# Performance work log

Measured on AMD Instinct MI355X. Metric: run time of the kernel, lower is better.

The kernel has to match this reference:

```python
import jax, jax.numpy as jnp
import numpy as np

N_ELEMENTS = 64  # StructureElementLayer(n_elements=64)


def setup_inputs() -> dict:
    key = jax.random.key(0)
    k1, k2 = jax.random.split(key)
    # x: [N, C, T, V] skeleton sequence (batch, coord channels, time, joints)
    x = jax.random.normal(k1, (256, 3, 256, 25), dtype=jnp.float32)
    # StructureElementLayer parameters (torch.rand init / ones*3 init)
    centres = jax.random.uniform(k2, (N_ELEMENTS, 2), dtype=jnp.float32)
    sharpness = jnp.ones((N_ELEMENTS, 2), dtype=jnp.float32) * 3.0
    return {"x": x, "centres": centres, "sharpness": sharpness}


def _mst_deaths(D):
    """Dim-0 Vietoris-Rips persistence deaths == MST edge weights (Prim's algorithm).

    D: [n, n] symmetric distance matrix. Returns [n-1] finite death values
    (births are all 0; the single essential (0, inf) pair contributes
    exp(-inf)=0 to the structure-element layer and is dropped).
    """
    n = D.shape[0]
    in_tree = jnp.zeros((n,), dtype=bool).at[0].set(True)
    dist = D[0]  # min distance from each node to the current tree

    def step(carry, _):
        in_tree, dist = carry
        d = jnp.where(in_tree, jnp.inf, dist)
        j = jnp.argmin(d)
        w = d[j]
        in_tree = in_tree.at[j].set(True)
        dist = jnp.minimum(dist, D[j])
        return (in_tree, dist), w

    (_, _), deaths = jax.lax.scan(step, (in_tree, dist), None, length=n - 1)
    return deaths


def _forward(x, centres, sharpness):
    xm = x.mean(1)                                  # [N, T, V]
    diff = xm[..., :, None] - xm[..., None, :]      # [N, T, V, V] pairwise joint diffs
    diff = diff.mean(-3)                            # [N, V, V]
    feat = jnp.linalg.norm(diff, axis=1)            # [N, V]  (torch.norm(., 2, dim=1))
    feat = (feat - feat.min()) / (feat.max() - feat.min())
    # Euclidean distance matrix of the N points in V-dim space (grad-safe sqrt)
    sq = jnp.sum(feat * feat, axis=1)
    D2 = sq[:, None] + sq[None, :] - 2.0 * (feat @ feat.T)
    D2 = jnp.maximum(D2, 0.0)
    D = jnp.where(D2 > 0.0, jnp.sqrt(jnp.where(D2 > 0.0, D2, 1.0)), 0.0)
    deaths = _mst_deaths(D)                         # [N-1]
    diag = jnp.stack([jnp.zeros_like(deaths), deaths], axis=-1)  # [N-1, 2] (birth, death)
    # StructureElementLayer: sum_i exp(-sum_d (p_id - c_kd)^2 * s_kd^2)
    d2 = (diag[:, None, :] - centres[None, :, :]) ** 2            # [N-1, K, 2]
    out = jnp.exp(-(d2 * (sharpness ** 2)).sum(-1)).sum(0)        # [K]
    return out


def reference(x, centres, sharpness):
    return _forward(x, centres, sharpness)
```

## Files before the change

kernel.cpp:

```cpp
#include <hip/hip_runtime.h>
#include <hip/hip_fp16.h>


#define WS_M    0
#define WS_MM   25600
#define WS_D16  65536

__global__ void k_mean(const float* __restrict__ x, float* __restrict__ m) {
    const int n = blockIdx.x;
    const int tid = threadIdx.x;
    __shared__ float sums[25];
    if (tid < 25) sums[tid] = 0.0f;
    __syncthreads();
    if (tid < 200) {
        const float* base = x + (long)n * 19200 + 4 * tid;
        float a0 = 0.f, a1 = 0.f, a2 = 0.f, a3 = 0.f;
        #pragma unroll
        for (int i = 0; i < 24; ++i) {
            float4 v = *reinterpret_cast<const float4*>(base + 800 * i);
            a0 += v.x; a1 += v.y; a2 += v.z; a3 += v.w;
        }
        const int v0 = (4 * tid) % 25;
        atomicAdd(&sums[v0], a0);
        atomicAdd(&sums[(v0 + 1) % 25], a1);
        atomicAdd(&sums[(v0 + 2) % 25], a2);
        atomicAdd(&sums[(v0 + 3) % 25], a3);
    }
    __syncthreads();
    if (tid < 25) m[n * 25 + tid] = sums[tid] * (1.0f / 768.0f);
}

__global__ void __launch_bounds__(256) k_dist(const float* __restrict__ m,
                                              unsigned short* __restrict__ D16,
                                              unsigned int* __restrict__ mm) {
    __shared__ float mS[6400];
    __shared__ float featS[6400];
    __shared__ unsigned int bmin, bmax;
    const int i = blockIdx.x;
    const int t = threadIdx.x;
    if (t == 0) { bmin = 0x7F800000u; bmax = 0u; }
    #pragma unroll
    for (int it = 0; it < 7; ++it) {
        int o = it * 256 + t;
        if (o < 1600) reinterpret_cast<float4*>(mS)[o] =
            reinterpret_cast<const float4*>(m)[o];
    }
    __syncthreads();
    float r[25];
    #pragma unroll
    for (int v = 0; v < 25; ++v) r[v] = mS[t * 25 + v];
    float S1 = 0.f, S2 = 0.f;
    #pragma unroll
    for (int v = 0; v < 25; ++v) { S1 += r[v]; S2 += r[v] * r[v]; }
    float fmn = 1e30f, fmx = -1e30f;
    #pragma unroll
    for (int w = 0; w < 25; ++w) {
        float q = S2 - 2.f * r[w] * S1 + 25.f * r[w] * r[w];
        q = fmaxf(q, 0.f);
        float f = sqrtf(q);
        featS[t * 25 + w] = f;
        fmn = fminf(fmn, f); fmx = fmaxf(fmx, f);
    }
    if (i == 0) {
        atomicMin(&bmin, __float_as_uint(fmn));
        atomicMax(&bmax, __float_as_uint(fmx));
    }
    __syncthreads();
    if (i == 0 && t == 0) { mm[0] = bmin; mm[1] = bmax; }
    float fi[25];
    #pragma unroll
    for (int v = 0; v < 25; ++v) fi[v] = featS[i * 25 + v];
    float s = 0.f;
    #pragma unroll
    for (int v = 0; v < 25; ++v) { float d = fi[v] - featS[t * 25 + v]; s += d * d; }
    D16[i * 256 + t] = __half_as_ushort(__float2half(s));
}

#define DSTR 264

__global__ void __launch_bounds__(256) k_mst(const unsigned short* __restrict__ D16g,
                                             const unsigned int* __restrict__ mm,
                                             const float* __restrict__ centres,
                                             const float* __restrict__ sharp,
                                             float* __restrict__ out) {
    __shared__ __align__(16) unsigned short Dl[256 * DSTR];
    __shared__ __align__(8) unsigned char compA[256];
    __shared__ unsigned char parent[256];
    __shared__ unsigned int compKey[256];
    __shared__ float deaths[256];
    __shared__ unsigned int dcount;
    __shared__ float outpart[256];
    const int tid = threadIdx.x;

    {
        const uint4* src = reinterpret_cast<const uint4*>(D16g);
        #pragma unroll
        for (int it = 0; it < 32; ++it) {
            const int flat = it * 256 + tid;
            const int r = flat >> 5, c = flat & 31;
            *reinterpret_cast<uint4*>(reinterpret_cast<char*>(Dl) + r * (DSTR * 2) + c * 16)
                = src[flat];
        }
    }
    compA[tid] = (unsigned char)tid;
    if (tid == 0) dcount = 0;
    __syncthreads();

    const int i = tid;
    const unsigned int ihi = (unsigned int)i << 8;
    const uint4* rowv = reinterpret_cast<const uint4*>(Dl + i * DSTR);
    const uint2* compv = reinterpret_cast<const uint2*>(compA);

    int nc = 256;
    while (nc > 1) {
        compKey[tid] = 0xFFFFFFFFu;
        __syncthreads();

        const unsigned int myComp = compA[i];
        unsigned int best = 0xFFFFFFFFu;
        #pragma unroll 4
        for (int c8 = 0; c8 < 32; ++c8) {
            const uint4 w4 = rowv[c8];
            const uint2 c2 = compv[c8];
            const int jb = c8 * 8;
            unsigned int wds[4] = {w4.x, w4.y, w4.z, w4.w};
            unsigned int cbs[2] = {c2.x, c2.y};
            #pragma unroll
            for (int u = 0; u < 8; ++u) {
                unsigned int w  = (wds[u >> 1] >> (16 * (u & 1))) & 0xFFFFu;
                unsigned int cj = (cbs[u >> 2] >> (8 * (u & 3))) & 0xFFu;
                unsigned int j = (unsigned int)(jb + u);
                unsigned int canon = (i < (int)j) ? (ihi | j) : ((j << 8) | (unsigned int)i);
                unsigned int key = (w << 16) | canon;
                key = (cj != myComp) ? key : 0xFFFFFFFFu;
                best = best < key ? best : key;
            }
        }
        if (best != 0xFFFFFFFFu) atomicMin(&compKey[myComp], best);
        __syncthreads();

        const unsigned int pk = compKey[tid];
        const bool isRoot = (compA[tid] == (unsigned char)tid);
        unsigned int par = (unsigned int)tid;
        if (isRoot && pk != 0xFFFFFFFFu) {
            const unsigned int canon = pk & 0xFFFFu;
            const unsigned int u = canon >> 8, v = canon & 0xFFu;
            const unsigned int cu = compA[u], cv = compA[v];
            par = (cu == (unsigned int)tid) ? cv : cu;
        }
        parent[tid] = (unsigned char)par;
        __syncthreads();

        if (isRoot && par != (unsigned int)tid) {
            if (parent[par] == (unsigned char)tid && (unsigned int)tid < par) {
                parent[tid] = (unsigned char)tid;
            } else {
                const unsigned int di = atomicAdd(&dcount, 1u);
                deaths[di] = sqrtf(__half2float(__ushort_as_half((unsigned short)(pk >> 16))));
            }
        }
        __syncthreads();

        #pragma unroll
        for (int s = 0; s < 8; ++s) {
            const unsigned char np = parent[parent[tid]];
            __syncthreads();
            parent[tid] = np;
            __syncthreads();
        }

        compA[tid] = parent[compA[tid]];
        nc = __syncthreads_count(compA[tid] == (unsigned char)tid);
    }

    const float mn = __uint_as_float(mm[0]);
    const float mx = __uint_as_float(mm[1]);
    const float inv = 1.0f / (mx - mn);
    const int k = tid & 63;
    const int part = tid >> 6;
    const float c0 = centres[2 * k], c1 = centres[2 * k + 1];
    const float s0 = sharp[2 * k],   s1 = sharp[2 * k + 1];
    const float t0 = c0 * c0 * s0 * s0;
    const float s1sq = s1 * s1;
    float acc = 0.f;
    for (int idx = part; idx < 255; idx += 4) {
        const float d = deaths[idx] * inv - c1;
        acc += __expf(-(t0 + d * d * s1sq));
    }
    outpart[tid] = acc;
    __syncthreads();
    if (tid < 64)
        out[tid] = outpart[tid] + outpart[tid + 64] + outpart[tid + 128] + outpart[tid + 192];
}

extern "C" void kernel_launch(void* const* d_in, const int* in_sizes, int n_in,
                              void* d_out, int out_size, void* d_ws, size_t ws_size,
                              hipStream_t stream) {
    const float* x       = (const float*)d_in[0];
    const float* centres = (const float*)d_in[1];
    const float* sharp   = (const float*)d_in[2];
    float* out = (float*)d_out;
    char* ws = (char*)d_ws;
    float*          m   = (float*)(ws + WS_M);
    unsigned int*   mm  = (unsigned int*)(ws + WS_MM);
    unsigned short* D16 = (unsigned short*)(ws + WS_D16);

    k_mean<<<256, 256, 0, stream>>>(x, m);
    k_dist<<<256, 256, 0, stream>>>(m, D16, mm);
    k_mst<<<1, 256, 0, stream>>>(D16, mm, centres, sharp, out);
}
```

Measured before the change: 107.3 us.

## Split Boruvka MST row scan across 1024 threads with precomputed edge keys

Runs the single-block MST kernel with 1024 threads: each row of the distance matrix is scanned by four threads, each covering 64 columns, and the per-row minima are combined through a two-stage atomicMin (row, then component). The canonical edge ids are precomputed once into registers instead of being rebuilt every round. Pointer jumping now stops early once the parents converge, instead of always running eight steps. The aim is to shorten the serial per-round scan in the latency-bound single-block kernel. In exchange it adds an extra sync and atomic stage per round and more register pressure at 1024 threads.

```diff
diff --git a/kernel.cpp b/kernel.cpp
--- a/kernel.cpp
+++ b/kernel.cpp
@@ -78,80 +78,103 @@
 
 #define DSTR 264
 
-__global__ void __launch_bounds__(256) k_mst(const unsigned short* __restrict__ D16g,
-                                             const unsigned int* __restrict__ mm,
-                                             const float* __restrict__ centres,
-                                             const float* __restrict__ sharp,
-                                             float* __restrict__ out) {
+__global__ void __launch_bounds__(1024) k_mst(const unsigned short* __restrict__ D16g,
+                                              const unsigned int* __restrict__ mm,
+                                              const float* __restrict__ centres,
+                                              const float* __restrict__ sharp,
+                                              float* __restrict__ out) {
     __shared__ __align__(16) unsigned short Dl[256 * DSTR];
     __shared__ __align__(8) unsigned char compA[256];
     __shared__ unsigned char parent[256];
+    __shared__ unsigned int rowKey[256];
     __shared__ unsigned int compKey[256];
     __shared__ float deaths[256];
     __shared__ unsigned int dcount;
-    __shared__ float outpart[256];
+    __shared__ float outpart[1024];
     const int tid = threadIdx.x;
 
     {
         const uint4* src = reinterpret_cast<const uint4*>(D16g);
         #pragma unroll
-        for (int it = 0; it < 32; ++it) {
-            const int flat = it * 256 + tid;
-            const int r = flat >> 5, c = flat & 31;
-            *reinterpret_cast<uint4*>(reinterpret_cast<char*>(Dl) + r * (DSTR * 2) + c * 16)
+        for (int it = 0; it < 8; ++it) {
+            const int flat = it * 1024 + tid;
+            const int rr = flat >> 5, cc = flat & 31;
+            *reinterpret_cast<uint4*>(reinterpret_cast<char*>(Dl) + rr * (DSTR * 2) + cc * 16)
                 = src[flat];
         }
     }
-    compA[tid] = (unsigned char)tid;
+    if (tid < 256) compA[tid] = (unsigned char)tid;
     if (tid == 0) dcount = 0;
     __syncthreads();
 
-    const int i = tid;
-    const unsigned int ihi = (unsigned int)i << 8;
-    const uint4* rowv = reinterpret_cast<const uint4*>(Dl + i * DSTR);
+    const int r = tid & 255;
+    const int q = tid >> 8;
+    const int jb0 = q * 64;
+    const uint4* rowq = reinterpret_cast<const uint4*>(
+        reinterpret_cast<const char*>(Dl) + r * (DSTR * 2) + jb0 * 2);
     const uint2* compv = reinterpret_cast<const uint2*>(compA);
+
+    unsigned int cano[32];
+    #pragma unroll
+    for (int t2 = 0; t2 < 32; ++t2) {
+        const int j0 = jb0 + 2 * t2, j1 = j0 + 1;
+        const unsigned int c0 = (r < j0) ? (((unsigned)r << 8) | j0) : (((unsigned)j0 << 8) | r);
+        const unsigned int c1 = (r < j1) ? (((unsigned)r << 8) | j1) : (((unsigned)j1 << 8) | r);
+        cano[t2] = c0 | (c1 << 16);
+    }
 
     int nc = 256;
     while (nc > 1) {
-        compKey[tid] = 0xFFFFFFFFu;
-        __syncthreads();
-
-        const unsigned int myComp = compA[i];
+        if (tid < 256) { rowKey[tid] = 0xFFFFFFFFu; compKey[tid] = 0xFFFFFFFFu; }
+        __syncthreads();
+
+        const unsigned int myComp = compA[r];
         unsigned int best = 0xFFFFFFFFu;
-        #pragma unroll 4
-        for (int c8 = 0; c8 < 32; ++c8) {
-            const uint4 w4 = rowv[c8];
-            const uint2 c2 = compv[c8];
-            const int jb = c8 * 8;
-            unsigned int wds[4] = {w4.x, w4.y, w4.z, w4.w};
-            unsigned int cbs[2] = {c2.x, c2.y};
+        #pragma unroll
+        for (int c8 = 0; c8 < 8; ++c8) {
+            const uint4 w4 = rowq[c8];
+            const uint2 c2 = compv[q * 8 + c8];
+            const unsigned int wds[4] = {w4.x, w4.y, w4.z, w4.w};
+            const unsigned int cbs[2] = {c2.x, c2.y};
             #pragma unroll
-            for (int u = 0; u < 8; ++u) {
-                unsigned int w  = (wds[u >> 1] >> (16 * (u & 1))) & 0xFFFFu;
-                unsigned int cj = (cbs[u >> 2] >> (8 * (u & 3))) & 0xFFu;
-                unsigned int j = (unsigned int)(jb + u);
-                unsigned int canon = (i < (int)j) ? (ihi | j) : ((j << 8) | (unsigned int)i);
-                unsigned int key = (w << 16) | canon;
-                key = (cj != myComp) ? key : 0xFFFFFFFFu;
-                best = best < key ? best : key;
+            for (int p = 0; p < 4; ++p) {
+                const unsigned int ww = wds[p];
+                const unsigned int cp = cano[c8 * 4 + p];
+                unsigned int k0 = (ww << 16) | (cp & 0xFFFFu);
+                unsigned int k1 = (ww & 0xFFFF0000u) | (cp >> 16);
+                const unsigned int cj0 = (cbs[p >> 1] >> (16 * (p & 1))) & 0xFFu;
+                const unsigned int cj1 = (cbs[p >> 1] >> (16 * (p & 1) + 8)) & 0xFFu;
+                k0 = (cj0 != myComp) ? k0 : 0xFFFFFFFFu;
+                k1 = (cj1 != myComp) ? k1 : 0xFFFFFFFFu;
+                best = best < k0 ? best : k0;
+                best = best < k1 ? best : k1;
             }
         }
-        if (best != 0xFFFFFFFFu) atomicMin(&compKey[myComp], best);
-        __syncthreads();
-
-        const unsigned int pk = compKey[tid];
-        const bool isRoot = (compA[tid] == (unsigned char)tid);
+        if (best != 0xFFFFFFFFu) atomicMin(&rowKey[r], best);
+        __syncthreads();
+        if (tid < 256) {
+            const unsigned int rk = rowKey[tid];
+            if (rk != 0xFFFFFFFFu) atomicMin(&compKey[compA[tid]], rk);
+        }
+        __syncthreads();
+
+        unsigned int pk = 0xFFFFFFFFu;
+        bool isRoot = false;
         unsigned int par = (unsigned int)tid;
-        if (isRoot && pk != 0xFFFFFFFFu) {
-            const unsigned int canon = pk & 0xFFFFu;
-            const unsigned int u = canon >> 8, v = canon & 0xFFu;
-            const unsigned int cu = compA[u], cv = compA[v];
-            par = (cu == (unsigned int)tid) ? cv : cu;
-        }
-        parent[tid] = (unsigned char)par;
-        __syncthreads();
-
-        if (isRoot && par != (unsigned int)tid) {
+        if (tid < 256) {
+            pk = compKey[tid];
+            isRoot = (compA[tid] == (unsigned char)tid);
+            if (isRoot && pk != 0xFFFFFFFFu) {
+                const unsigned int canon = pk & 0xFFFFu;
+                const unsigned int u = canon >> 8, v = canon & 0xFFu;
+                const unsigned int cu = compA[u], cv = compA[v];
+                par = (cu == (unsigned int)tid) ? cv : cu;
+            }
+            parent[tid] = (unsigned char)par;
+        }
+        __syncthreads();
+
+        if (tid < 256 && isRoot && par != (unsigned int)tid) {
             if (parent[par] == (unsigned char)tid && (unsigned int)tid < par) {
                 parent[tid] = (unsigned char)tid;
             } else {
@@ -161,16 +184,17 @@
         }
         __syncthreads();
 
-        #pragma unroll
-        for (int s = 0; s < 8; ++s) {
-            const unsigned char np = parent[parent[tid]];
+        for (;;) {
+            unsigned char p0 = 0, np = 0;
+            if (tid < 256) { p0 = parent[tid]; np = parent[p0]; }
+            const int cnt = __syncthreads_count(tid < 256 && np != p0);
+            if (tid < 256) parent[tid] = np;
             __syncthreads();
-            parent[tid] = np;
-            __syncthreads();
-        }
-
-        compA[tid] = parent[compA[tid]];
-        nc = __syncthreads_count(compA[tid] == (unsigned char)tid);
+            if (cnt == 0) break;
+        }
+
+        if (tid < 256) compA[tid] = parent[compA[tid]];
+        nc = __syncthreads_count(tid < 256 && compA[tid] == (unsigned char)tid);
     }
 
     const float mn = __uint_as_float(mm[0]);
@@ -183,14 +207,18 @@
     const float t0 = c0 * c0 * s0 * s0;
     const float s1sq = s1 * s1;
     float acc = 0.f;
-    for (int idx = part; idx < 255; idx += 4) {
+    for (int idx = part; idx < 255; idx += 16) {
         const float d = deaths[idx] * inv - c1;
         acc += __expf(-(t0 + d * d * s1sq));
     }
     outpart[tid] = acc;
     __syncthreads();
-    if (tid < 64)
-        out[tid] = outpart[tid] + outpart[tid + 64] + outpart[tid + 128] + outpart[tid + 192];
+    if (tid < 64) {
+        float s = 0.f;
+        #pragma unroll
+        for (int pp = 0; pp < 16; ++pp) s += outpart[tid + 64 * pp];
+        out[tid] = s;
+    }
 }
 
 extern "C" void kernel_launch(void* const* d_in, const int* in_sizes, int n_in,
@@ -207,5 +235,5 @@
 
     k_mean<<<256, 256, 0, stream>>>(x, m);
     k_dist<<<256, 256, 0, stream>>>(m, D16, mm);
-    k_mst<<<1, 256, 0, stream>>>(D16, mm, centres, sharp, out);
-}
+    k_mst<<<1, 1024, 0, stream>>>(D16, mm, centres, sharp, out);
+}
```

New measurement: 98.26 us. -8.4%, faster.
